# Kernel tuning notes

Measured on AMD Instinct MI355X. Metric: run time of the kernel, lower is better.

The kernel has to match this reference:

```python
import jax, jax.numpy as jnp
import numpy as np

B = 48            # graph pairs
NQ, NC = 20, 16   # query / corpus node counts (corpus padded to NMAX)
NMAX = 20         # max_node_set_size
DN, DE = 16, 8    # raw node / edge feature dims
D = 32            # node_state_dim
EH = 64           # edge_hidden_sizes[-1]
EQ, EC = 80, 60   # edges per query / corpus graph
PROP = 5          # n_prop_layers
TEMP = 0.01       # sinkhorn temperature
ITERS = 20        # sinkhorn iterations
LAMBDA = 1.0
NTOT = B * (NQ + NC)
NE = B * (EQ + EC)
SRC, DST = np.triu_indices(NMAX, 1)   # nC2 = 190 node pairs
_indq = np.ones(NMAX, np.int32)
_indc = np.array([1] * NC + [0] * (NMAX - NC), np.int32)
NXOR = jnp.asarray((_indq[:, None] ^ _indc[None, :]).astype(np.float32))  # [20,20]


def _mlp2(x, w1, b1, w2, b2):
    return jnp.maximum(x @ w1 + b1, 0.0) @ w2 + b2


def _sinkhorn(log_alpha):
    la = log_alpha / TEMP
    for _ in range(ITERS):
        la = la - jax.nn.logsumexp(la, axis=2, keepdims=True)
        la = la - jax.nn.logsumexp(la, axis=1, keepdims=True)
    return jnp.exp(la)


def _edge_emb(H, adj, w1, b1, w2, b2):
    s, d = H[:, SRC], H[:, DST]            # [B,nC2,D] gathers
    e = adj[:, SRC, DST][..., None]        # [B,nC2,1]
    f = _mlp2(jnp.concatenate([s, d, e], -1), w1, b1, w2, b2)
    bk = _mlp2(jnp.concatenate([d, s, e], -1), w1, b1, w2, b2)
    return f + bk                          # bidirectional msg, [B,nC2,EH]


def _forward(node_features, edge_features, query_adj, corpus_adj,
             enc_nw, enc_nb, enc_ew, enc_eb,
             msg_w1, msg_b1, msg_w2, msg_b2,
             upd_w1, upd_b1, upd_w2, upd_b2,
             sink_w1, sink_b1, sink_w2, sink_b2,
             lrl_w1, lrl_b1, lrl_w2, lrl_b2,
             from_idx, to_idx):
    h = node_features @ enc_nw + enc_nb    # GMN encoder (linear MLPs)
    e = edge_features @ enc_ew + enc_eb
    for _ in range(PROP):                  # shared-param propagation
        msg = _mlp2(jnp.concatenate([h[from_idx], h[to_idx], e], -1),
                    msg_w1, msg_b1, msg_w2, msg_b2)
        agg = jax.ops.segment_sum(msg, to_idx, num_segments=NTOT)
        h = h + _mlp2(jnp.concatenate([agg, h], -1), upd_w1, upd_b1, upd_w2, upd_b2)
    hp = h.reshape(B, NQ + NC, D)          # split_and_stack (static sizes)
    Hq = hp[:, :NQ]
    Hc = jnp.pad(hp[:, NQ:], ((0, 0), (0, NMAX - NC), (0, 0)))
    tq = _mlp2(Hq, sink_w1, sink_b1, sink_w2, sink_b2)
    tc = _mlp2(Hc, sink_w1, sink_b1, sink_w2, sink_b2)
    cost = jnp.abs(tq[:, :, None, :] - tc[:, None, :, :]).sum(-1)  # cdist p=1
    P = _sinkhorn(-cost)                   # node transport plan [B,20,20]
    Eq = _edge_emb(Hq, query_adj, lrl_w1, lrl_b1, lrl_w2, lrl_b2)
    Ec = _edge_emb(Hc, corpus_adj, lrl_w1, lrl_b1, lrl_w2, lrl_b2)
    Pa, Pb = P[:, SRC, :], P[:, DST, :]
    straight = Pa[:, :, SRC] * Pb[:, :, DST]    # plan[src_i,src_j]*plan[dst_i,dst_j]
    cross = Pa[:, :, DST] * Pb[:, :, SRC]
    eT = straight + cross                  # use_max=False, no second sinkhorn
    aq = query_adj[:, SRC, DST].astype(jnp.int32)
    ac = corpus_adj[:, SRC, DST].astype(jnp.int32)
    pxor = (aq[:, :, None] ^ ac[:, None, :]).astype(P.dtype)
    ediff = Eq[:, :, None, :] - Ec[:, None, :, :]   # [B,nC2,nC2,EH]
    ecost = jnp.maximum(ediff, 0.0).sum(-1) + jnp.maximum(-ediff, 0.0).sum(-1)
    edge_align = (pxor * eT * ecost).sum((-1, -2))
    ndiff = Hq[:, :, None, :] - Hc[:, None, :, :]   # [B,20,20,D]
    ncost = jnp.maximum(ndiff, 0.0).sum(-1) + jnp.maximum(-ndiff, 0.0).sum(-1)
    node_align = (NXOR * P * ncost).sum((-1, -2))
    return edge_align + LAMBDA * node_align         # [B]


def setup_inputs():
    key = jax.random.key(0)
    rng = np.random.default_rng(0)
    base = (np.arange(B) * (NQ + NC))[:, None]
    fq = base + rng.integers(0, NQ, (B, EQ)); tq = base + rng.integers(0, NQ, (B, EQ))
    fc = base + NQ + rng.integers(0, NC, (B, EC)); tc = base + NQ + rng.integers(0, NC, (B, EC))
    from_idx = jnp.asarray(np.concatenate([fq, fc], 1).reshape(-1), jnp.int32)
    to_idx = jnp.asarray(np.concatenate([tq, tc], 1).reshape(-1), jnp.int32)
    qadj = rng.integers(0, 2, (B, NMAX, NMAX)).astype(np.float32)
    cadj = rng.integers(0, 2, (B, NMAX, NMAX)).astype(np.float32)
    cadj[:, NC:, :] = 0.0; cadj[:, :, NC:] = 0.0   # padded corpus nodes have no edges
    ks = iter(jax.random.split(key, 32))
    def w(shape, s=0.1):
        return jax.random.normal(next(ks), shape, jnp.float32) * s
    return {
        'node_features': w((NTOT, DN), 1.0),
        'edge_features': w((NE, DE), 1.0),
        'query_adj': jnp.asarray(qadj),
        'corpus_adj': jnp.asarray(cadj),
        'enc_nw': w((DN, D)), 'enc_nb': w((D,)),
        'enc_ew': w((DE, 16)), 'enc_eb': w((16,)),
        'msg_w1': w((2 * D + 16, EH)), 'msg_b1': w((EH,)),
        'msg_w2': w((EH, EH)), 'msg_b2': w((EH,)),
        'upd_w1': w((EH + D, EH)), 'upd_b1': w((EH,)),
        'upd_w2': w((EH, D)), 'upd_b2': w((D,)),
        'sink_w1': w((D, NMAX)), 'sink_b1': w((NMAX,)),
        'sink_w2': w((NMAX, NMAX)), 'sink_b2': w((NMAX,)),
        'lrl_w1': w((2 * D + 1, EH)), 'lrl_b1': w((EH,)),
        'lrl_w2': w((EH, EH)), 'lrl_b2': w((EH,)),
        'from_idx': from_idx, 'to_idx': to_idx,
        'graph_sizes': jnp.asarray(np.tile([NQ, NC], B), jnp.int32),
    }


def reference(node_features, edge_features, query_adj, corpus_adj,
              enc_nw, enc_nb, enc_ew, enc_eb,
              msg_w1, msg_b1, msg_w2, msg_b2,
              upd_w1, upd_b1, upd_w2, upd_b2,
              sink_w1, sink_b1, sink_w2, sink_b2,
              lrl_w1, lrl_b1, lrl_w2, lrl_b2,
              from_idx, to_idx, graph_sizes):
    return _forward(node_features, edge_features, query_adj, corpus_adj,
                    enc_nw, enc_nb, enc_ew, enc_eb,
                    msg_w1, msg_b1, msg_w2, msg_b2,
                    upd_w1, upd_b1, upd_w2, upd_b2,
                    sink_w1, sink_b1, sink_w2, sink_b2,
                    lrl_w1, lrl_b1, lrl_w2, lrl_b2,
                    from_idx, to_idx)
```

## Files before the change

### kernel.cpp

```cpp
#include <hip/hip_runtime.h>


constexpr int kB    = 48;
constexpr int kNM   = 20;
constexpr int kD    = 32;
constexpr int kNP   = 190;
constexpr int kNTOT = 1728;
constexpr int kIters = 20;
constexpr float kInvT = 100.0f;

__device__ __forceinline__ void pair_sd(int p, int& s, int& d) {
    int row = 0, rem = p;
    #pragma unroll
    for (int r = 0; r < 19; ++r) {
        int len = 19 - r;
        if (rem < len) { row = r; break; }
        rem -= len;
    }
    s = row; d = row + 1 + rem;
}

__device__ __forceinline__ float bc(float v, int k) {
    return __int_as_float(__builtin_amdgcn_readlane(__float_as_int(v), k));
}

__device__ __forceinline__ void lse20(float (&r)[20]) {
    float m01 = fmaxf(r[0], r[1]),  m23 = fmaxf(r[2], r[3]),
          m45 = fmaxf(r[4], r[5]),  m67 = fmaxf(r[6], r[7]),
          m89 = fmaxf(r[8], r[9]),  mab = fmaxf(r[10], r[11]),
          mcd = fmaxf(r[12], r[13]), mef = fmaxf(r[14], r[15]),
          mgh = fmaxf(r[16], r[17]), mij = fmaxf(r[18], r[19]);
    float n0 = fmaxf(m01, m23), n1 = fmaxf(m45, m67), n2 = fmaxf(m89, mab),
          n3 = fmaxf(mcd, mef), n4 = fmaxf(mgh, mij);
    float m = fmaxf(fmaxf(fmaxf(n0, n1), fmaxf(n2, n3)), n4);
    float e[20];
    #pragma unroll
    for (int k = 0; k < 20; ++k) e[k] = __expf(r[k] - m);
    float s01 = e[0] + e[1],  s23 = e[2] + e[3],  s45 = e[4] + e[5],
          s67 = e[6] + e[7],  s89 = e[8] + e[9],  sab = e[10] + e[11],
          scd = e[12] + e[13], sef = e[14] + e[15], sgh = e[16] + e[17],
          sij = e[18] + e[19];
    float t0 = s01 + s23, t1 = s45 + s67, t2 = s89 + sab,
          t3 = scd + sef, t4 = sgh + sij;
    float s = ((t0 + t1) + (t2 + t3)) + t4;
    float l = m + __logf(s);
    #pragma unroll
    for (int k = 0; k < 20; ++k) r[k] -= l;
}

__global__ void k_enc(const float* __restrict__ nf, const float* __restrict__ nw,
                      const float* __restrict__ nb, const float* __restrict__ ef,
                      const float* __restrict__ ew, const float* __restrict__ eb,
                      float* __restrict__ h, float* __restrict__ ee,
                      float* __restrict__ agg, float* __restrict__ out) {
    int tid = blockIdx.x * 256 + threadIdx.x;
    int stride = gridDim.x * 256;
    for (int i = tid; i < kNTOT * 32; i += stride) {
        int n = i >> 5, c = i & 31;
        float acc = nb[c];
        const float* row = nf + n * 16;
        #pragma unroll
        for (int k = 0; k < 16; ++k) acc = fmaf(row[k], nw[k * 32 + c], acc);
        h[i] = acc;
    }
    for (int i = tid; i < 6720 * 16; i += stride) {
        int n = i >> 4, c = i & 15;
        float acc = eb[c];
        const float* row = ef + n * 8;
        #pragma unroll
        for (int k = 0; k < 8; ++k) acc = fmaf(row[k], ew[k * 16 + c], acc);
        ee[i] = acc;
    }
    for (int i = tid; i < kNTOT * 64; i += stride) agg[i] = 0.f;
    if (tid < kB) out[tid] = 0.f;
}

__global__ void __launch_bounds__(256)
k_msg(const float* __restrict__ h, const float* __restrict__ ee,
      const int* __restrict__ fidx, const int* __restrict__ tidx,
      const float* __restrict__ w1, const float* __restrict__ b1,
      const float* __restrict__ w2, const float* __restrict__ b2,
      float* __restrict__ agg) {
    int w = threadIdx.x >> 6, lane = threadIdx.x & 63;
    int e0 = (blockIdx.x * 4 + w) * 2;
    int toj[2]; float xa[2], xb[2], acc[2], o[2];
    #pragma unroll
    for (int j = 0; j < 2; ++j) {
        int e = e0 + j;
        int fr = fidx[e]; toj[j] = tidx[e];
        xa[j] = h[(lane < 32 ? fr : toj[j]) * kD + (lane & 31)];
        xb[j] = ee[e * 16 + (lane & 15)];
        acc[j] = b1[lane];
    }
    #pragma unroll
    for (int k = 0; k < 64; ++k) {
        float w1k = w1[k * 64 + lane];
        #pragma unroll
        for (int j = 0; j < 2; ++j) acc[j] = fmaf(bc(xa[j], k), w1k, acc[j]);
    }
    #pragma unroll
    for (int k = 0; k < 16; ++k) {
        float w1k = w1[(64 + k) * 64 + lane];
        #pragma unroll
        for (int j = 0; j < 2; ++j) acc[j] = fmaf(bc(xb[j], k), w1k, acc[j]);
    }
    #pragma unroll
    for (int j = 0; j < 2; ++j) { acc[j] = fmaxf(acc[j], 0.f); o[j] = b2[lane]; }
    #pragma unroll
    for (int k = 0; k < 64; ++k) {
        float w2k = w2[k * 64 + lane];
        #pragma unroll
        for (int j = 0; j < 2; ++j) o[j] = fmaf(bc(acc[j], k), w2k, o[j]);
    }
    #pragma unroll
    for (int j = 0; j < 2; ++j) atomicAdd(&agg[toj[j] * 64 + lane], o[j]);
}

__global__ void __launch_bounds__(256)
k_upd(float* __restrict__ h, float* __restrict__ agg,
      const float* __restrict__ w1, const float* __restrict__ b1,
      const float* __restrict__ w2, const float* __restrict__ b2) {
    int w = threadIdx.x >> 6, lane = threadIdx.x & 63;
    int n0 = (blockIdx.x * 4 + w) * 2;
    float xa[2], xb[2], acc[2], o[2];
    #pragma unroll
    for (int j = 0; j < 2; ++j) {
        int n = n0 + j;
        xa[j] = agg[n * 64 + lane];
        agg[n * 64 + lane] = 0.f;
        xb[j] = h[n * kD + (lane & 31)];
        acc[j] = b1[lane];
    }
    #pragma unroll
    for (int k = 0; k < 64; ++k) {
        float w1k = w1[k * 64 + lane];
        #pragma unroll
        for (int j = 0; j < 2; ++j) acc[j] = fmaf(bc(xa[j], k), w1k, acc[j]);
    }
    #pragma unroll
    for (int k = 0; k < 32; ++k) {
        float w1k = w1[(64 + k) * 64 + lane];
        #pragma unroll
        for (int j = 0; j < 2; ++j) acc[j] = fmaf(bc(xb[j], k), w1k, acc[j]);
    }
    #pragma unroll
    for (int j = 0; j < 2; ++j) { acc[j] = fmaxf(acc[j], 0.f); o[j] = b2[lane & 31]; }
    #pragma unroll
    for (int k = 0; k < 64; ++k) {
        float w2k = w2[k * 32 + (lane & 31)];
        #pragma unroll
        for (int j = 0; j < 2; ++j) o[j] = fmaf(bc(acc[j], k), w2k, o[j]);
    }
    if (lane < 32) {
        #pragma unroll
        for (int j = 0; j < 2; ++j) h[(n0 + j) * kD + lane] += o[j];
    }
}

__global__ void k_sink_t(const float* __restrict__ h,
                         const float* __restrict__ w1, const float* __restrict__ b1,
                         const float* __restrict__ w2, const float* __restrict__ b2,
                         float* __restrict__ Hq, float* __restrict__ Hc,
                         float* __restrict__ tq, float* __restrict__ tc) {
    __shared__ float xs[4][32];
    __shared__ float hs[4][20];
    int w = threadIdx.x >> 6, lane = threadIdx.x & 63;
    int xcd = blockIdx.x & 7, slot = blockIdx.x >> 3;
    int b = xcd + 8 * (slot / 10);
    int task = (slot % 10) * 4 + w;
    int side = task >= 20;
    int i = task - side * 20;
    if (lane < 32) {
        float v;
        if (side == 0) v = h[(b * 36 + i) * kD + lane];
        else           v = (i < 16) ? h[(b * 36 + 20 + i) * kD + lane] : 0.f;
        (side ? Hc : Hq)[(b * kNM + i) * kD + lane] = v;
        xs[w][lane] = v;
    }
    __syncthreads();
    if (lane < kNM) {
        float acc = b1[lane];
        #pragma unroll
        for (int k = 0; k < kD; ++k) acc += xs[w][k] * w1[k * kNM + lane];
        hs[w][lane] = fmaxf(acc, 0.f);
    }
    __syncthreads();
    if (lane < kNM) {
        float o = b2[lane];
        #pragma unroll
        for (int k = 0; k < kNM; ++k) o += hs[w][k] * w2[k * kNM + lane];
        (side ? tc : tq)[(b * kNM + i) * kNM + lane] = o;
    }
}

__global__ void k_sinkhorn(const float* __restrict__ tq, const float* __restrict__ tc,
                           const float* __restrict__ Hq,
                           float* __restrict__ P, float* __restrict__ out) {
    __shared__ float tcS[400];
    __shared__ float tr[20 * 21];
    int b = blockIdx.x, lane = threadIdx.x;
    for (int i = lane; i < 400; i += 64) tcS[i] = tc[b * 400 + i];
    int i20 = lane < 20 ? lane : 0;
    float tqr[20];
    #pragma unroll
    for (int k = 0; k < 20; ++k) tqr[k] = tq[(b * 20 + i20) * 20 + k];
    __syncthreads();
    float r[20];
    #pragma unroll
    for (int j = 0; j < 20; ++j) {
        float c = 0.f;
        #pragma unroll
        for (int k = 0; k < 20; ++k) c += fabsf(tqr[k] - tcS[j * 20 + k]);
        r[j] = -c * kInvT;
    }
    for (int it = 0; it < kIters; ++it) {
        lse20(r);
        if (lane < 20) {
            #pragma unroll
            for (int j = 0; j < 20; ++j) tr[lane * 21 + j] = r[j];
        }
        __syncthreads();
        if (lane < 20) {
            #pragma unroll
            for (int i = 0; i < 20; ++i) r[i] = tr[i * 21 + lane];
        }
        __syncthreads();
        lse20(r);
        if (lane < 20) {
            #pragma unroll
            for (int i = 0; i < 20; ++i) tr[i * 21 + lane] = r[i];
        }
        __syncthreads();
        if (lane < 20) {
            #pragma unroll
            for (int j = 0; j < 20; ++j) r[j] = tr[lane * 21 + j];
        }
        __syncthreads();
    }
    float part = 0.f;
    if (lane < 20) {
        float pv[20];
        #pragma unroll
        for (int j = 0; j < 20; ++j) pv[j] = __expf(r[j]);
        float* Pb = P + b * 400 + lane * 20;
        #pragma unroll
        for (int j = 0; j < 20; ++j) Pb[j] = pv[j];
        float pr4 = (pv[16] + pv[17]) + (pv[18] + pv[19]);
        float l1 = 0.f;
        const float* hq = Hq + (b * 20 + lane) * 32;
        #pragma unroll
        for (int k = 0; k < 32; ++k) l1 += fabsf(hq[k]);
        part = pr4 * l1;
    }
    #pragma unroll
    for (int off = 32; off; off >>= 1) part += __shfl_down(part, off, 64);
    if (lane == 0) atomicAdd(&out[b], part);
}

__global__ void __launch_bounds__(256)
k_edge_emb(const float* __restrict__ Hq, const float* __restrict__ Hc,
           const float* __restrict__ qadj, const float* __restrict__ cadj,
           const float* __restrict__ w1, const float* __restrict__ b1,
           const float* __restrict__ w2, const float* __restrict__ b2,
           float* __restrict__ Eq, float* __restrict__ Ec) {
    int w = threadIdx.x >> 6, lane = threadIdx.x & 63;
    int xcd = blockIdx.x & 7, slot = blockIdx.x >> 3;
    int b = xcd + 8 * (slot / 24);
    int r = slot % 24;
    float xa[4], ev[4], af[4], ab[4];
    int sidej[4], pj[4];
    #pragma unroll
    for (int j = 0; j < 4; ++j) {
        int tloc = r * 16 + w * 4 + j;
        if (tloc >= 380) tloc = 379;
        sidej[j] = tloc / kNP; pj[j] = tloc % kNP;
        int s, d; pair_sd(pj[j], s, d);
        const float* H = sidej[j] ? Hc : Hq;
        xa[j] = (lane < 32) ? H[(b * kNM + s) * kD + lane]
                            : H[(b * kNM + d) * kD + (lane - 32)];
        ev[j] = (sidej[j] ? cadj : qadj)[b * 400 + s * 20 + d];
        float bb = b1[lane];
        af[j] = bb; ab[j] = bb;
    }
    #pragma unroll
    for (int k = 0; k < 64; ++k) {
        float w1k = w1[k * 64 + lane];
        #pragma unroll
        for (int j = 0; j < 4; ++j) {
            af[j] = fmaf(bc(xa[j], k),      w1k, af[j]);
            ab[j] = fmaf(bc(xa[j], k ^ 32), w1k, ab[j]);
        }
    }
    {
        float w1e = w1[64 * 64 + lane];
        #pragma unroll
        for (int j = 0; j < 4; ++j) {
            af[j] = fmaf(ev[j], w1e, af[j]);
            ab[j] = fmaf(ev[j], w1e, ab[j]);
        }
    }
    float hid[4], o[4];
    #pragma unroll
    for (int j = 0; j < 4; ++j) {
        hid[j] = fmaxf(af[j], 0.f) + fmaxf(ab[j], 0.f);
        o[j] = 2.f * b2[lane];
    }
    #pragma unroll
    for (int k = 0; k < 64; ++k) {
        float w2k = w2[k * 64 + lane];
        #pragma unroll
        for (int j = 0; j < 4; ++j) o[j] = fmaf(bc(hid[j], k), w2k, o[j]);
    }
    #pragma unroll
    for (int j = 0; j < 4; ++j)
        (sidej[j] ? Ec : Eq)[(b * kNP + pj[j]) * 64 + lane] = o[j];
}

#define EC_ALL(X) X(0) X(1) X(2) X(3) X(4) X(5) X(6) X(7) X(8) X(9) X(10) X(11) \
  X(12) X(13) X(14) X(15) X(16) X(17) X(18) X(19) X(20) X(21) X(22) X(23) \
  X(24) X(25) X(26) X(27) X(28) X(29) X(30) X(31)

__global__ void __launch_bounds__(256, 4)
k_final(const float* __restrict__ P, const float* __restrict__ Eq,
        const float* __restrict__ Ec, const float* __restrict__ qadj,
        const float* __restrict__ cadj, float* __restrict__ out) {
    __shared__ float Ps[400];
    __shared__ unsigned char spsh[192], dpsh[192];
    int xcd = blockIdx.x & 7, slot = blockIdx.x >> 3;
    int b = xcd + 8 * (slot / 6), qt = slot % 6;
    int t = threadIdx.x, w = t >> 6, lane = t & 63;

    int l31 = lane & 31;
    int q = qt * 32 + l31;
    bool qv = q < kNP;
    int sqe = 0, dqe = 0;
    { int qc = qv ? q : 0; pair_sd(qc, sqe, dqe); }
    float acv = qv ? cadj[b * 400 + sqe * 20 + dqe] : 0.f;
    const float* ecb = Ec + (b * kNP + qt * 32) * 64 + lane;
#define EC_DECL(i) float ec##i = (qt * 32 + i < kNP) ? ecb[i * 64] : 0.f;
    EC_ALL(EC_DECL)
#undef EC_DECL

    if (t < 192) {
        int s = 0, d = 0;
        if (t < kNP) pair_sd(t, s, d);
        spsh[t] = (unsigned char)s;
        dpsh[t] = (unsigned char)d;
    }
    for (int i = t; i < 400; i += 256) Ps[i] = P[b * 400 + i];
    __syncthreads();

    int sq = sqe, dq = dqe;

    float a0 = 0.f, a1 = 0.f, a2 = 0.f, a3 = 0.f;
    int pp = w;
    float aqc = qadj[b * 400 + spsh[pp] * 20 + dpsh[pp]];
    float eqc = Eq[(b * kNP + pp) * 64 + lane];
    while (pp < kNP) {
        int pn = pp + 4;
        float aqn = 0.f, eqn = 0.f;
        if (pn < kNP) {
            aqn = qadj[b * 400 + spsh[pn] * 20 + dpsh[pn]];
            eqn = Eq[(b * kNP + pn) * 64 + lane];
        }
        int sp = spsh[pp], dp = dpsh[pp];
        float eT = Ps[sp * 20 + sq] * Ps[dp * 20 + dq]
                 + Ps[sp * 20 + dq] * Ps[dp * 20 + sq];
        float wqv = qv ? ((aqc > 0.5f) ? (1.f - acv) : acv) * eT : 0.f;
#define EC_FMA(i) { float d_ = fabsf(eqc - ec##i); \
        if ((i & 3) == 0) a0 = fmaf(bc(wqv, i), d_, a0); \
        else if ((i & 3) == 1) a1 = fmaf(bc(wqv, i), d_, a1); \
        else if ((i & 3) == 2) a2 = fmaf(bc(wqv, i), d_, a2); \
        else a3 = fmaf(bc(wqv, i), d_, a3); }
        EC_ALL(EC_FMA)
#undef EC_FMA
        aqc = aqn; eqc = eqn; pp = pn;
    }
    float partial = (a0 + a1) + (a2 + a3);
    #pragma unroll
    for (int off = 32; off; off >>= 1) partial += __shfl_down(partial, off, 64);
    if (lane == 0) atomicAdd(&out[b], partial);
}

extern "C" void kernel_launch(void* const* d_in, const int* in_sizes, int n_in,
                              void* d_out, int out_size, void* d_ws, size_t ws_size,
                              hipStream_t stream) {
    auto f = [&](int i) { return (const float*)d_in[i]; };
    const float* nf   = f(0);
    const float* ef   = f(1);
    const float* qadj = f(2);
    const float* cadj = f(3);
    const int* from_idx = (const int*)d_in[24];
    const int* to_idx   = (const int*)d_in[25];
    float* out = (float*)d_out;

    float* ws  = (float*)d_ws;
    float* h   = ws;
    float* ee  = h   + 55296;
    float* agg = ee  + 107520;
    float* Hq  = agg + 110592;
    float* Hc  = Hq  + 30720;
    float* tq  = Hc  + 30720;
    float* tc  = tq  + 19200;
    float* P   = tc  + 19200;
    float* Eq  = P   + 19200;
    float* Ec  = Eq  + 583680;

    k_enc<<<432, 256, 0, stream>>>(nf, f(4), f(5), ef, f(6), f(7), h, ee, agg, out);
    for (int it = 0; it < 5; ++it) {
        k_msg<<<840, 256, 0, stream>>>(h, ee, from_idx, to_idx,
                                       f(8), f(9), f(10), f(11), agg);
        k_upd<<<216, 256, 0, stream>>>(h, agg, f(12), f(13), f(14), f(15));
    }
    k_sink_t<<<480, 256, 0, stream>>>(h, f(16), f(17), f(18), f(19), Hq, Hc, tq, tc);
    k_sinkhorn<<<48, 64, 0, stream>>>(tq, tc, Hq, P, out);
    k_edge_emb<<<1152, 256, 0, stream>>>(Hq, Hc, qadj, cadj,
                                         f(20), f(21), f(22), f(23), Eq, Ec);
    k_final<<<288, 256, 0, stream>>>(P, Eq, Ec, qadj, cadj, out);
}
```

Before: 151.0 us.

## Fuse sinkhorn transform and edge embedding into one launch, drop Hq/Hc staging

Merges the sinkhorn feature-transform kernel and the edge-embedding kernel into a single k_mid launch, with block ranges picking the role. Both now read node states straight from h, so the padded Hq/Hc staging copies are gone and sinkhorn reads h directly. This saves one kernel launch and the intermediate writes and reads. The cost is a heterogeneous grid whose register use is set by the heavier edge-MLP path.

```diff
diff --git a/kernel.cpp b/kernel.cpp
--- a/kernel.cpp
+++ b/kernel.cpp
@@ -157,44 +157,106 @@
     }
 }
 
-__global__ void k_sink_t(const float* __restrict__ h,
-                         const float* __restrict__ w1, const float* __restrict__ b1,
-                         const float* __restrict__ w2, const float* __restrict__ b2,
-                         float* __restrict__ Hq, float* __restrict__ Hc,
-                         float* __restrict__ tq, float* __restrict__ tc) {
+__global__ void __launch_bounds__(256)
+k_mid(const float* __restrict__ h,
+      const float* __restrict__ qadj, const float* __restrict__ cadj,
+      const float* __restrict__ sw1, const float* __restrict__ sb1,
+      const float* __restrict__ sw2, const float* __restrict__ sb2,
+      const float* __restrict__ lw1, const float* __restrict__ lb1,
+      const float* __restrict__ lw2, const float* __restrict__ lb2,
+      float* __restrict__ tq, float* __restrict__ tc,
+      float* __restrict__ Eq, float* __restrict__ Ec) {
     __shared__ float xs[4][32];
     __shared__ float hs[4][20];
     int w = threadIdx.x >> 6, lane = threadIdx.x & 63;
-    int xcd = blockIdx.x & 7, slot = blockIdx.x >> 3;
-    int b = xcd + 8 * (slot / 10);
-    int task = (slot % 10) * 4 + w;
-    int side = task >= 20;
-    int i = task - side * 20;
-    if (lane < 32) {
+
+    if (blockIdx.x < 480) {
+        int xcd = blockIdx.x & 7, slot = blockIdx.x >> 3;
+        int b = xcd + 8 * (slot / 10);
+        int task = (slot % 10) * 4 + w;
+        int side = task >= 20;
+        int i = task - side * 20;
+        if (lane < 32) {
+            float v;
+            if (side == 0) v = h[(b * 36 + i) * kD + lane];
+            else           v = (i < 16) ? h[(b * 36 + 20 + i) * kD + lane] : 0.f;
+            xs[w][lane] = v;
+        }
+        __syncthreads();
+        if (lane < kNM) {
+            float acc = sb1[lane];
+            #pragma unroll
+            for (int k = 0; k < kD; ++k) acc += xs[w][k] * sw1[k * kNM + lane];
+            hs[w][lane] = fmaxf(acc, 0.f);
+        }
+        __syncthreads();
+        if (lane < kNM) {
+            float o = sb2[lane];
+            #pragma unroll
+            for (int k = 0; k < kNM; ++k) o += hs[w][k] * sw2[k * kNM + lane];
+            (side ? tc : tq)[(b * kNM + i) * kNM + lane] = o;
+        }
+        return;
+    }
+
+    int bid = blockIdx.x - 480;
+    int xcd = bid & 7, slot = bid >> 3;
+    int b = xcd + 8 * (slot / 24);
+    int r = slot % 24;
+    float xa[4], ev[4], af[4], ab[4];
+    int sidej[4], pj[4];
+    #pragma unroll
+    for (int j = 0; j < 4; ++j) {
+        int tloc = r * 16 + w * 4 + j;
+        if (tloc >= 380) tloc = 379;
+        sidej[j] = tloc / kNP; pj[j] = tloc % kNP;
+        int s, d; pair_sd(pj[j], s, d);
+        int rr = (lane < 32) ? s : d;
+        int cc = lane & 31;
         float v;
-        if (side == 0) v = h[(b * 36 + i) * kD + lane];
-        else           v = (i < 16) ? h[(b * 36 + 20 + i) * kD + lane] : 0.f;
-        (side ? Hc : Hq)[(b * kNM + i) * kD + lane] = v;
-        xs[w][lane] = v;
-    }
-    __syncthreads();
-    if (lane < kNM) {
-        float acc = b1[lane];
-        #pragma unroll
-        for (int k = 0; k < kD; ++k) acc += xs[w][k] * w1[k * kNM + lane];
-        hs[w][lane] = fmaxf(acc, 0.f);
-    }
-    __syncthreads();
-    if (lane < kNM) {
-        float o = b2[lane];
-        #pragma unroll
-        for (int k = 0; k < kNM; ++k) o += hs[w][k] * w2[k * kNM + lane];
-        (side ? tc : tq)[(b * kNM + i) * kNM + lane] = o;
-    }
+        if (!sidej[j]) v = h[(b * 36 + rr) * kD + cc];
+        else           v = (rr < 16) ? h[(b * 36 + 20 + rr) * kD + cc] : 0.f;
+        xa[j] = v;
+        ev[j] = (sidej[j] ? cadj : qadj)[b * 400 + s * 20 + d];
+        float bb = lb1[lane];
+        af[j] = bb; ab[j] = bb;
+    }
+    #pragma unroll
+    for (int k = 0; k < 64; ++k) {
+        float w1k = lw1[k * 64 + lane];
+        #pragma unroll
+        for (int j = 0; j < 4; ++j) {
+            af[j] = fmaf(bc(xa[j], k),      w1k, af[j]);
+            ab[j] = fmaf(bc(xa[j], k ^ 32), w1k, ab[j]);
+        }
+    }
+    {
+        float w1e = lw1[64 * 64 + lane];
+        #pragma unroll
+        for (int j = 0; j < 4; ++j) {
+            af[j] = fmaf(ev[j], w1e, af[j]);
+            ab[j] = fmaf(ev[j], w1e, ab[j]);
+        }
+    }
+    float hid[4], o[4];
+    #pragma unroll
+    for (int j = 0; j < 4; ++j) {
+        hid[j] = fmaxf(af[j], 0.f) + fmaxf(ab[j], 0.f);
+        o[j] = 2.f * lb2[lane];
+    }
+    #pragma unroll
+    for (int k = 0; k < 64; ++k) {
+        float w2k = lw2[k * 64 + lane];
+        #pragma unroll
+        for (int j = 0; j < 4; ++j) o[j] = fmaf(bc(hid[j], k), w2k, o[j]);
+    }
+    #pragma unroll
+    for (int j = 0; j < 4; ++j)
+        (sidej[j] ? Ec : Eq)[(b * kNP + pj[j]) * 64 + lane] = o[j];
 }
 
 __global__ void k_sinkhorn(const float* __restrict__ tq, const float* __restrict__ tc,
-                           const float* __restrict__ Hq,
+                           const float* __restrict__ h,
                            float* __restrict__ P, float* __restrict__ out) {
     __shared__ float tcS[400];
     __shared__ float tr[20 * 21];
@@ -247,7 +309,7 @@
         for (int j = 0; j < 20; ++j) Pb[j] = pv[j];
         float pr4 = (pv[16] + pv[17]) + (pv[18] + pv[19]);
         float l1 = 0.f;
-        const float* hq = Hq + (b * 20 + lane) * 32;
+        const float* hq = h + (b * 36 + lane) * kD;
         #pragma unroll
         for (int k = 0; k < 32; ++k) l1 += fabsf(hq[k]);
         part = pr4 * l1;
@@ -255,65 +317,6 @@
     #pragma unroll
     for (int off = 32; off; off >>= 1) part += __shfl_down(part, off, 64);
     if (lane == 0) atomicAdd(&out[b], part);
-}
-
-__global__ void __launch_bounds__(256)
-k_edge_emb(const float* __restrict__ Hq, const float* __restrict__ Hc,
-           const float* __restrict__ qadj, const float* __restrict__ cadj,
-           const float* __restrict__ w1, const float* __restrict__ b1,
-           const float* __restrict__ w2, const float* __restrict__ b2,
-           float* __restrict__ Eq, float* __restrict__ Ec) {
-    int w = threadIdx.x >> 6, lane = threadIdx.x & 63;
-    int xcd = blockIdx.x & 7, slot = blockIdx.x >> 3;
-    int b = xcd + 8 * (slot / 24);
-    int r = slot % 24;
-    float xa[4], ev[4], af[4], ab[4];
-    int sidej[4], pj[4];
-    #pragma unroll
-    for (int j = 0; j < 4; ++j) {
-        int tloc = r * 16 + w * 4 + j;
-        if (tloc >= 380) tloc = 379;
-        sidej[j] = tloc / kNP; pj[j] = tloc % kNP;
-        int s, d; pair_sd(pj[j], s, d);
-        const float* H = sidej[j] ? Hc : Hq;
-        xa[j] = (lane < 32) ? H[(b * kNM + s) * kD + lane]
-                            : H[(b * kNM + d) * kD + (lane - 32)];
-        ev[j] = (sidej[j] ? cadj : qadj)[b * 400 + s * 20 + d];
-        float bb = b1[lane];
-        af[j] = bb; ab[j] = bb;
-    }
-    #pragma unroll
-    for (int k = 0; k < 64; ++k) {
-        float w1k = w1[k * 64 + lane];
-        #pragma unroll
-        for (int j = 0; j < 4; ++j) {
-            af[j] = fmaf(bc(xa[j], k),      w1k, af[j]);
-            ab[j] = fmaf(bc(xa[j], k ^ 32), w1k, ab[j]);
-        }
-    }
-    {
-        float w1e = w1[64 * 64 + lane];
-        #pragma unroll
-        for (int j = 0; j < 4; ++j) {
-            af[j] = fmaf(ev[j], w1e, af[j]);
-            ab[j] = fmaf(ev[j], w1e, ab[j]);
-        }
-    }
-    float hid[4], o[4];
-    #pragma unroll
-    for (int j = 0; j < 4; ++j) {
-        hid[j] = fmaxf(af[j], 0.f) + fmaxf(ab[j], 0.f);
-        o[j] = 2.f * b2[lane];
-    }
-    #pragma unroll
-    for (int k = 0; k < 64; ++k) {
-        float w2k = w2[k * 64 + lane];
-        #pragma unroll
-        for (int j = 0; j < 4; ++j) o[j] = fmaf(bc(hid[j], k), w2k, o[j]);
-    }
-    #pragma unroll
-    for (int j = 0; j < 4; ++j)
-        (sidej[j] ? Ec : Eq)[(b * kNP + pj[j]) * 64 + lane] = o[j];
 }
 
 #define EC_ALL(X) X(0) X(1) X(2) X(3) X(4) X(5) X(6) X(7) X(8) X(9) X(10) X(11) \
@@ -398,9 +401,7 @@
     float* h   = ws;
     float* ee  = h   + 55296;
     float* agg = ee  + 107520;
-    float* Hq  = agg + 110592;
-    float* Hc  = Hq  + 30720;
-    float* tq  = Hc  + 30720;
+    float* tq  = agg + 110592;
     float* tc  = tq  + 19200;
     float* P   = tc  + 19200;
     float* Eq  = P   + 19200;
@@ -412,9 +413,10 @@
                                        f(8), f(9), f(10), f(11), agg);
         k_upd<<<216, 256, 0, stream>>>(h, agg, f(12), f(13), f(14), f(15));
     }
-    k_sink_t<<<480, 256, 0, stream>>>(h, f(16), f(17), f(18), f(19), Hq, Hc, tq, tc);
-    k_sinkhorn<<<48, 64, 0, stream>>>(tq, tc, Hq, P, out);
-    k_edge_emb<<<1152, 256, 0, stream>>>(Hq, Hc, qadj, cadj,
-                                         f(20), f(21), f(22), f(23), Eq, Ec);
+    k_mid<<<1632, 256, 0, stream>>>(h, qadj, cadj,
+                                    f(16), f(17), f(18), f(19),
+                                    f(20), f(21), f(22), f(23),
+                                    tq, tc, Eq, Ec);
+    k_sinkhorn<<<48, 64, 0, stream>>>(tq, tc, h, P, out);
     k_final<<<288, 256, 0, stream>>>(P, Eq, Ec, qadj, cadj, out);
 }
```

Result: no change. 151.0 us (-0.0%).
